# Performance work log

Measured on AMD Instinct MI355X. Metric: run time of the kernel, lower is better.

The kernel has to match this reference:

```python
import jax, jax.numpy as jnp
import numpy as np

N, DEG, D_FEAT, D_OUT = 50000, 32, 128, 256

def setup_inputs() -> dict:
    key = jax.random.key(0)
    k1, k2, k3 = jax.random.split(key, 3)
    features = jax.random.normal(k1, (N, D_FEAT), dtype=jnp.float32)
    edge_look_up = jax.random.randint(k2, (N, DEG), 0, N, dtype=jnp.int64)
    # glorot-uniform kernel, shape (2*D_FEAT, D_OUT)
    limit = np.sqrt(6.0 / (2 * D_FEAT + D_OUT)).astype(np.float32)
    kernel = jax.random.uniform(k3, (2 * D_FEAT, D_OUT), dtype=jnp.float32,
                                minval=-limit, maxval=limit)
    return {"features": features, "edge_look_up": edge_look_up, "kernel": kernel}

def reference(features, edge_look_up, kernel):
    # [1] neighborhood aggregation: gather neighbor features and mean-reduce
    neigh = features[edge_look_up]          # [N, DEG, D_FEAT] (irregular gather)
    agg = jnp.mean(neigh, axis=1)           # [N, D_FEAT]
    # [2] concat self features with aggregated neighbor vectors
    out = jnp.concatenate([features, agg], axis=-1)  # [N, 2*D_FEAT]
    # [4] dense matmul + [5] relu activation
    return jax.nn.relu(out @ kernel)        # [N, D_OUT]
```

## Files before the change

kernel.cpp:

```cpp
#include <hip/hip_runtime.h>

#define NN  50000
#define DEG 32
#define DF  128
#define DO  256
#define FEAT4 (NN * DF / 4)

typedef __bf16 bf16x8 __attribute__((ext_vector_type(8)));
typedef float  f32x4  __attribute__((ext_vector_type(4)));
typedef float  f32x2  __attribute__((ext_vector_type(2)));
typedef unsigned short u16x8 __attribute__((ext_vector_type(8)));

#if defined(__has_builtin)
#if __has_builtin(__builtin_amdgcn_cvt_pk_f32_fp8) && __has_builtin(__builtin_amdgcn_cvt_pk_fp8_f32)
#define HW_FP8 1
#endif
#endif
#ifndef HW_FP8
#define HW_FP8 0
#endif

__device__ __forceinline__ unsigned short f2bf(float f) {
    unsigned u = __float_as_uint(f);
    u += 0x7FFF + ((u >> 16) & 1);
    return (unsigned short)(u >> 16);
}

#if !HW_FP8
__device__ __forceinline__ unsigned enc1_fp8(float f) {
    unsigned u = __float_as_uint(f);
    unsigned s = (u >> 31) << 7;
    float a = fabsf(f);
    if (!(a > 0.f)) return s;
    if (a >= 448.f) return s | 0x7E;
    u = __float_as_uint(a);
    int e = (int)((u >> 23) & 255) - 127;
    if (e < -6) {
        unsigned m = (unsigned)(a * 512.f + 0.5f);
        if (m >= 8) return s | 0x08;
        return s | m;
    }
    unsigned mant = (u >> 20) & 7;
    unsigned rnd  = ((u >> 19) & 1) & (((u & 0x7FFFF) != 0) | ((u >> 20) & 1));
    unsigned enc  = ((unsigned)(e + 7) << 3) | mant;
    return s | (enc + rnd);
}
__device__ __forceinline__ float dec1_fp8(unsigned b) {
    unsigned s = (b >> 7) & 1, e = (b >> 3) & 15, m = b & 7;
    float v = (e == 0) ? (float)m * 0.001953125f
                       : __uint_as_float(((e - 7 + 127) << 23) | (m << 20));
    return s ? -v : v;
}
#endif

__device__ __forceinline__ unsigned enc4_fp8(float4 v) {
#if HW_FP8
    int pk = 0;
    pk = __builtin_amdgcn_cvt_pk_fp8_f32(v.x, v.y, pk, false);
    pk = __builtin_amdgcn_cvt_pk_fp8_f32(v.z, v.w, pk, true);
    return (unsigned)pk;
#else
    return enc1_fp8(v.x) | (enc1_fp8(v.y) << 8) | (enc1_fp8(v.z) << 16) | (enc1_fp8(v.w) << 24);
#endif
}

__global__ __launch_bounds__(256) void convert_kernel(
    const float* __restrict__ feat, const float* __restrict__ W,
    unsigned* __restrict__ feat8, unsigned short* __restrict__ Wt)
{
    const int gid = blockIdx.x * 256 + threadIdx.x;
    if (gid < FEAT4) {
        const float4 v = ((const float4*)feat)[gid];
        feat8[gid] = enc4_fp8(v);
    } else {
        const int t = gid - FEAT4;
        if (t < DO * DO) {
            const int n = t >> 8, k = t & 255;
            Wt[n * DO + k] = f2bf(W[k * DO + n]);
        }
    }
}

__global__ __launch_bounds__(256) void agg_kernel(
    const unsigned* __restrict__ feat8,
    const int*      __restrict__ edges,
    unsigned short* __restrict__ aggb)
{
    const int node = blockIdx.x * 16 + (threadIdx.x >> 4);
    const int l    = threadIdx.x & 15;
    const int* e   = edges + node * DEG;

    float a[8] = {0.f, 0.f, 0.f, 0.f, 0.f, 0.f, 0.f, 0.f};
    #pragma unroll
    for (int d = 0; d < DEG; ++d) {
        const int idx = e[d];
        const uint2 pk = *(const uint2*)(feat8 + (size_t)idx * (DF / 4) + l * 2);
#if HW_FP8
        const f32x2 v0 = __builtin_amdgcn_cvt_pk_f32_fp8((int)pk.x, false);
        const f32x2 v1 = __builtin_amdgcn_cvt_pk_f32_fp8((int)pk.x, true);
        const f32x2 v2 = __builtin_amdgcn_cvt_pk_f32_fp8((int)pk.y, false);
        const f32x2 v3 = __builtin_amdgcn_cvt_pk_f32_fp8((int)pk.y, true);
        a[0] += v0[0]; a[1] += v0[1]; a[2] += v1[0]; a[3] += v1[1];
        a[4] += v2[0]; a[5] += v2[1]; a[6] += v3[0]; a[7] += v3[1];
#else
        #pragma unroll
        for (int j = 0; j < 4; ++j) a[j]     += dec1_fp8((pk.x >> (8 * j)) & 255);
        #pragma unroll
        for (int j = 0; j < 4; ++j) a[4 + j] += dec1_fp8((pk.y >> (8 * j)) & 255);
#endif
    }

    const float s = 1.0f / (float)DEG;
    u16x8 o;
    #pragma unroll
    for (int j = 0; j < 8; ++j) o[j] = f2bf(a[j] * s);
    *(u16x8*)(aggb + (size_t)node * DF + l * 8) = o;
}

#define BM  32
#define BN  256
#define LDT 72

__global__ __launch_bounds__(256) void gemm_kernel(
    const float*          __restrict__ feat,
    const unsigned short* __restrict__ aggb,
    const unsigned short* __restrict__ Wt,
    float*                __restrict__ out)
{
    __shared__ __align__(16) unsigned short Asw[BM * LDT];
    __shared__ __align__(16) unsigned short Bsw[BN * LDT];

    const int tid = threadIdx.x;
    const int m0  = blockIdx.x * BM;

    const int wave = tid >> 6, lane = tid & 63;
    const int quad = lane >> 4, lr = lane & 15;
    const int wn   = wave * 64;

    const int kstart = blockIdx.x & 3;

    f32x4 acc[2][4] = {};

    for (int j = 0; j < 4; ++j) {
        const int kc = (kstart + j) & 3;

        if (j) __syncthreads();

        {
            const int r = tid >> 3;
            const int c = (tid & 7) * 8;
            int node = m0 + r;
            if (node >= NN) node = NN - 1;
            if (kc < 2) {
                const float* src = feat + (size_t)node * DF + kc * 64 + c;
                const float4 v0 = *(const float4*)(src);
                const float4 v1 = *(const float4*)(src + 4);
                u16x8 o;
                o[0] = f2bf(v0.x); o[1] = f2bf(v0.y); o[2] = f2bf(v0.z); o[3] = f2bf(v0.w);
                o[4] = f2bf(v1.x); o[5] = f2bf(v1.y); o[6] = f2bf(v1.z); o[7] = f2bf(v1.w);
                *(u16x8*)(Asw + r * LDT + c) = o;
            } else {
                *(u16x8*)(Asw + r * LDT + c) =
                    *(const u16x8*)(aggb + (size_t)node * DF + (kc - 2) * 64 + c);
            }
        }

        #pragma unroll
        for (int it = 0; it < 8; ++it) {
            const int sidx = it * 256 + tid;
            const int r = sidx >> 3;
            const int c = (sidx & 7) * 8;
            *(u16x8*)(Bsw + r * LDT + c) =
                *(const u16x8*)(Wt + (size_t)r * DO + kc * 64 + c);
        }

        __syncthreads();

        #pragma unroll
        for (int kk = 0; kk < 64; kk += 32) {
            const int kb = kk + quad * 8;
            bf16x8 af[2], bfr[4];
            #pragma unroll
            for (int i = 0; i < 2; ++i)
                af[i] = *(const bf16x8*)(Asw + (i * 16 + lr) * LDT + kb);
            #pragma unroll
            for (int i = 0; i < 4; ++i)
                bfr[i] = *(const bf16x8*)(Bsw + (wn + i * 16 + lr) * LDT + kb);
            #pragma unroll
            for (int mi = 0; mi < 2; ++mi)
                #pragma unroll
                for (int ni = 0; ni < 4; ++ni)
                    acc[mi][ni] = __builtin_amdgcn_mfma_f32_16x16x32_bf16(
                        af[mi], bfr[ni], acc[mi][ni], 0, 0, 0);
        }
    }

    #pragma unroll
    for (int mi = 0; mi < 2; ++mi) {
        #pragma unroll
        for (int r = 0; r < 4; ++r) {
            const int row = m0 + mi * 16 + quad * 4 + r;
            if (row < NN) {
                #pragma unroll
                for (int ni = 0; ni < 4; ++ni) {
                    out[(size_t)row * DO + wn + ni * 16 + lr] =
                        fmaxf(acc[mi][ni][r], 0.f);
                }
            }
        }
    }
}

extern "C" void kernel_launch(void* const* d_in, const int* in_sizes, int n_in,
                              void* d_out, int out_size, void* d_ws, size_t ws_size,
                              hipStream_t stream)
{
    const float* feat  = (const float*)d_in[0];
    const int*   edges = (const int*)d_in[1];
    const float* W     = (const float*)d_in[2];
    float*       out   = (float*)d_out;

    unsigned short* aggb  = (unsigned short*)d_ws;
    unsigned*       feat8 = (unsigned*)(aggb + (size_t)NN * DF);
    unsigned short* Wt    = (unsigned short*)(feat8 + (size_t)NN * DF / 4);

    convert_kernel<<<(FEAT4 + DO * DO + 255) / 256, 256, 0, stream>>>(
        feat, W, feat8, Wt);
    agg_kernel<<<NN / 16, 256, 0, stream>>>(feat8, edges, aggb);

    gemm_kernel<<<(NN + BM - 1) / BM, 256, 0, stream>>>(feat, aggb, Wt, out);
}
```

Baseline: 124.8 us.

## Double GEMM row tile, use direct global-to-LDS loads with XOR swizzle

The GEMM block grows to 64 rows and 512 threads with a 2x4 wave grid, so each staged 256x64 weight tile feeds twice as many output rows and B-tile traffic is halved. The weight and aggregated-feature tiles are now copied straight into LDS with global_load_lds instead of going through registers. The padded LDS layout is replaced by an XOR-swizzled unpadded layout to avoid bank conflicts. Larger blocks mean fewer blocks for tail balancing, and the direct-to-LDS path depends on how the builtin maps lanes to LDS addresses.

```diff
diff --git a/kernel.cpp b/kernel.cpp
--- a/kernel.cpp
+++ b/kernel.cpp
@@ -64,6 +64,12 @@
 #endif
 }
 
+__device__ __forceinline__ void gload_lds16(const void* g, void* l) {
+    __builtin_amdgcn_global_load_lds(
+        (const __attribute__((address_space(1))) unsigned int*)g,
+        (__attribute__((address_space(3))) unsigned int*)l, 16, 0, 0);
+}
+
 __global__ __launch_bounds__(256) void convert_kernel(
     const float* __restrict__ feat, const float* __restrict__ W,
     unsigned* __restrict__ feat8, unsigned short* __restrict__ Wt)
@@ -117,27 +123,33 @@
     *(u16x8*)(aggb + (size_t)node * DF + l * 8) = o;
 }
 
-#define BM  32
+#define BM  64
 #define BN  256
-#define LDT 72
-
-__global__ __launch_bounds__(256) void gemm_kernel(
+
+__global__ __launch_bounds__(512) void gemm_kernel(
     const float*          __restrict__ feat,
     const unsigned short* __restrict__ aggb,
     const unsigned short* __restrict__ Wt,
     float*                __restrict__ out)
 {
-    __shared__ __align__(16) unsigned short Asw[BM * LDT];
-    __shared__ __align__(16) unsigned short Bsw[BN * LDT];
+    __shared__ __align__(16) unsigned short Asw[BM * 64];
+    __shared__ __align__(16) unsigned short Bsw[BN * 64];
 
     const int tid = threadIdx.x;
     const int m0  = blockIdx.x * BM;
 
     const int wave = tid >> 6, lane = tid & 63;
     const int quad = lane >> 4, lr = lane & 15;
-    const int wn   = wave * 64;
+    const int wm   = (wave & 1) * 32;
+    const int wn   = (wave >> 1) * 64;
 
     const int kstart = blockIdx.x & 3;
+
+    const int r  = tid >> 3;
+    const int s  = tid & 7;
+    const int gsA = s ^ (r & 7);
+    int nodeA = m0 + r;
+    if (nodeA >= NN) nodeA = NN - 1;
 
     f32x4 acc[2][4] = {};
 
@@ -146,46 +158,45 @@
 
         if (j) __syncthreads();
 
-        {
-            const int r = tid >> 3;
-            const int c = (tid & 7) * 8;
-            int node = m0 + r;
-            if (node >= NN) node = NN - 1;
-            if (kc < 2) {
-                const float* src = feat + (size_t)node * DF + kc * 64 + c;
-                const float4 v0 = *(const float4*)(src);
-                const float4 v1 = *(const float4*)(src + 4);
-                u16x8 o;
-                o[0] = f2bf(v0.x); o[1] = f2bf(v0.y); o[2] = f2bf(v0.z); o[3] = f2bf(v0.w);
-                o[4] = f2bf(v1.x); o[5] = f2bf(v1.y); o[6] = f2bf(v1.z); o[7] = f2bf(v1.w);
-                *(u16x8*)(Asw + r * LDT + c) = o;
-            } else {
-                *(u16x8*)(Asw + r * LDT + c) =
-                    *(const u16x8*)(aggb + (size_t)node * DF + (kc - 2) * 64 + c);
-            }
-        }
-
-        #pragma unroll
-        for (int it = 0; it < 8; ++it) {
-            const int sidx = it * 256 + tid;
-            const int r = sidx >> 3;
-            const int c = (sidx & 7) * 8;
-            *(u16x8*)(Bsw + r * LDT + c) =
-                *(const u16x8*)(Wt + (size_t)r * DO + kc * 64 + c);
+        if (kc < 2) {
+            const float* src = feat + (size_t)nodeA * DF + kc * 64 + gsA * 8;
+            const float4 v0 = *(const float4*)(src);
+            const float4 v1 = *(const float4*)(src + 4);
+            u16x8 o;
+            o[0] = f2bf(v0.x); o[1] = f2bf(v0.y); o[2] = f2bf(v0.z); o[3] = f2bf(v0.w);
+            o[4] = f2bf(v1.x); o[5] = f2bf(v1.y); o[6] = f2bf(v1.z); o[7] = f2bf(v1.w);
+            *(u16x8*)(Asw + r * 64 + s * 8) = o;
+        } else {
+            gload_lds16(aggb + (size_t)nodeA * DF + (kc - 2) * 64 + gsA * 8,
+                        Asw + r * 64 + s * 8);
+        }
+
+        #pragma unroll
+        for (int it = 0; it < 4; ++it) {
+            const int sidx = it * 512 + tid;
+            const int br = sidx >> 3;
+            const int bs = sidx & 7;
+            const int gs = bs ^ (br & 7);
+            gload_lds16(Wt + (size_t)br * DO + kc * 64 + gs * 8,
+                        Bsw + br * 64 + bs * 8);
         }
 
         __syncthreads();
 
         #pragma unroll
         for (int kk = 0; kk < 64; kk += 32) {
-            const int kb = kk + quad * 8;
+            const int G = (kk >> 3) + quad;
             bf16x8 af[2], bfr[4];
             #pragma unroll
-            for (int i = 0; i < 2; ++i)
-                af[i] = *(const bf16x8*)(Asw + (i * 16 + lr) * LDT + kb);
+            for (int i = 0; i < 2; ++i) {
+                const int R = wm + i * 16 + lr;
+                af[i] = *(const bf16x8*)(Asw + R * 64 + ((G ^ (R & 7)) << 3));
+            }
             #pragma unroll
-            for (int i = 0; i < 4; ++i)
-                bfr[i] = *(const bf16x8*)(Bsw + (wn + i * 16 + lr) * LDT + kb);
+            for (int i = 0; i < 4; ++i) {
+                const int R = wn + i * 16 + lr;
+                bfr[i] = *(const bf16x8*)(Bsw + R * 64 + ((G ^ (R & 7)) << 3));
+            }
             #pragma unroll
             for (int mi = 0; mi < 2; ++mi)
                 #pragma unroll
@@ -198,13 +209,13 @@
     #pragma unroll
     for (int mi = 0; mi < 2; ++mi) {
         #pragma unroll
-        for (int r = 0; r < 4; ++r) {
-            const int row = m0 + mi * 16 + quad * 4 + r;
+        for (int rr = 0; rr < 4; ++rr) {
+            const int row = m0 + wm + mi * 16 + quad * 4 + rr;
             if (row < NN) {
                 #pragma unroll
                 for (int ni = 0; ni < 4; ++ni) {
                     out[(size_t)row * DO + wn + ni * 16 + lr] =
-                        fmaxf(acc[mi][ni][r], 0.f);
+                        fmaxf(acc[mi][ni][rr], 0.f);
                 }
             }
         }
@@ -228,5 +239,5 @@
         feat, W, feat8, Wt);
     agg_kernel<<<NN / 16, 256, 0, stream>>>(feat8, edges, aggb);
 
-    gemm_kernel<<<(NN + BM - 1) / BM, 256, 0, stream>>>(feat, aggb, Wt, out);
-}
+    gemm_kernel<<<(NN + BM - 1) / BM, 512, 0, stream>>>(feat, aggb, Wt, out);
+}
```

After: 124.0 us. About the same (-0.7%).
